# Performance work log

Hardware: AMD Instinct MI355X
Metric: run time of the kernel (lower is better)

Reference implementation:

```python
import jax, jax.numpy as jnp
import numpy as np

N_NODES = 100000
N_EDGES = 3200000
D = 128


def setup_inputs() -> dict:
    key = jax.random.key(0)
    ks = jax.random.split(key, 6)
    x = jax.random.normal(ks[0], (N_NODES, D), dtype=jnp.float32)
    w = jax.random.uniform(ks[1], (N_EDGES,), dtype=jnp.float32)
    W = jax.random.normal(ks[2], (D, D), dtype=jnp.float32) * (1.0 / np.sqrt(D))
    b = jax.random.normal(ks[3], (D,), dtype=jnp.float32) * 0.01
    src = jax.random.randint(ks[4], (N_EDGES,), 0, N_NODES, dtype=jnp.int64)
    dst = jax.random.randint(ks[5], (N_EDGES,), 0, N_NODES, dtype=jnp.int64)
    return {"x": x, "w": w, "W": W, "b": b, "src": src, "dst": dst}


def reference(x, w, W, b, src, dst):
    # h = linear(x)  -> [N, D]
    h = x @ W.T + b
    # u_mul_e: gather source features, scale by per-edge weight  -> [E, D]
    m = h[src] * w[:, None]
    # sum aggregation at destinations (SpMM scatter-add)  -> [N, D]
    out = jax.ops.segment_sum(m, dst, num_segments=N_NODES)
    return out
```

## Files before the change

kernel.cpp:

```cpp
#include <hip/hip_runtime.h>
#include <hip/hip_fp16.h>

constexpr int N_NODES = 100000;
constexpr int N_EDGES = 3200000;
constexpr int NB2 = (N_NODES + 63) >> 6;
constexpr int LCAP = 2432;
constexpr int TILE = 8192;
constexpr int NTILES = (N_EDGES + TILE - 1) / TILE;

__global__ __launch_bounds__(256) void cvt_kernel(const float* __restrict__ x,
                                                  __half* __restrict__ xh) {
  const int stride = gridDim.x * 256;
  const int total = N_NODES * 128 / 4;
  for (int i = blockIdx.x * 256 + threadIdx.x; i < total; i += stride) {
    float4 v = ((const float4*)x)[i];
    __half2 a = __floats2half2_rn(v.x, v.y);
    __half2 b = __floats2half2_rn(v.z, v.w);
    ((__half2*)xh)[2 * i] = a;
    ((__half2*)xh)[2 * i + 1] = b;
  }
}

__global__ __launch_bounds__(256) void bin3_kernel(
    const int* __restrict__ src, const int* __restrict__ dst,
    const float* __restrict__ w, int* __restrict__ gtail,
    int2* __restrict__ lists) {
  __shared__ int lcnt[NB2];
  __shared__ int lbase[NB2];
  const int t = threadIdx.x;
  const int e0 = blockIdx.x * TILE;
  const int n = min(TILE, N_EDGES - e0);

  for (int i = t; i < NB2; i += 256) lcnt[i] = 0;
  __syncthreads();

  for (int off = t; off < n; off += 256)
    atomicAdd(&lcnt[(dst[e0 + off] >> 6)], 1);
  __syncthreads();

  for (int i = t; i < NB2; i += 256) {
    int c = lcnt[i];
    lbase[i] = (c > 0) ? atomicAdd(&gtail[i], c) : 0;
    lcnt[i] = 0;
  }
  __syncthreads();

  for (int off = t; off < n; off += 256) {
    int e = e0 + off;
    int d = dst[e];
    int l = d >> 6;
    int p = lbase[l] + atomicAdd(&lcnt[l], 1);
    if ((unsigned)p < (unsigned)LCAP)
      lists[(size_t)l * LCAP + p] =
          make_int2(src[e] | ((d & 63) << 17), __float_as_int(w[e]));
  }
}

__global__ __launch_bounds__(256) void agg4_kernel(
    const __half* __restrict__ xh, const int2* __restrict__ lists,
    const int* __restrict__ gtail, float* __restrict__ agg_out,
    float* __restrict__ sw) {
  __shared__ int2 sorted[LCAP];
  __shared__ int rcnt[64], roff[65], rcur[64];
  const int b = blockIdx.x;
  const int t = threadIdx.x;
  const int c = min(gtail[b], LCAP);
  const int2* base = lists + (size_t)b * LCAP;

  if (t < 64) rcnt[t] = 0;
  __syncthreads();

  for (int j = t; j < c; j += 256)
    atomicAdd(&rcnt[(base[j].x >> 17) & 63], 1);
  __syncthreads();

  if (t < 64) {
    int v = rcnt[t];
    int inc = v;
    #pragma unroll
    for (int d = 1; d < 64; d <<= 1) {
      int u = __shfl_up(inc, d, 64);
      if (t >= d) inc += u;
    }
    roff[t] = inc - v;
    rcur[t] = inc - v;
    if (t == 63) roff[64] = inc;
  }
  __syncthreads();

  for (int j = t; j < c; j += 256) {
    int2 r = base[j];
    int p = atomicAdd(&rcur[(r.x >> 17) & 63], 1);
    if ((unsigned)p < (unsigned)LCAP) sorted[p] = r;
  }
  __syncthreads();

  const int wv = t >> 6, lane = t & 63;
  const int nd = min(64, N_NODES - b * 64);
  const __half2* xh2 = (const __half2*)xh;
  for (int ri = 0; ri < 16; ++ri) {
    int r = wv * 16 + ri;
    int j0 = min(roff[r], c), j1 = min(roff[r + 1], c);
    float2 acc = make_float2(0.f, 0.f);
    float sws = 0.f;
    int j = j0;
    for (; j + 8 <= j1; j += 8) {
      int2 e0 = sorted[j];
      int2 e1 = sorted[j + 1];
      int2 e2 = sorted[j + 2];
      int2 e3 = sorted[j + 3];
      int2 e4 = sorted[j + 4];
      int2 e5 = sorted[j + 5];
      int2 e6 = sorted[j + 6];
      int2 e7 = sorted[j + 7];
      __half2 h0 = xh2[(size_t)(e0.x & 0x1FFFF) * 64 + lane];
      __half2 h1 = xh2[(size_t)(e1.x & 0x1FFFF) * 64 + lane];
      __half2 h2 = xh2[(size_t)(e2.x & 0x1FFFF) * 64 + lane];
      __half2 h3 = xh2[(size_t)(e3.x & 0x1FFFF) * 64 + lane];
      __half2 h4 = xh2[(size_t)(e4.x & 0x1FFFF) * 64 + lane];
      __half2 h5 = xh2[(size_t)(e5.x & 0x1FFFF) * 64 + lane];
      __half2 h6 = xh2[(size_t)(e6.x & 0x1FFFF) * 64 + lane];
      __half2 h7 = xh2[(size_t)(e7.x & 0x1FFFF) * 64 + lane];
      float2 v0 = __half22float2(h0);
      float2 v1 = __half22float2(h1);
      float2 v2 = __half22float2(h2);
      float2 v3 = __half22float2(h3);
      float2 v4 = __half22float2(h4);
      float2 v5 = __half22float2(h5);
      float2 v6 = __half22float2(h6);
      float2 v7 = __half22float2(h7);
      float w0 = __int_as_float(e0.y), w1 = __int_as_float(e1.y);
      float w2 = __int_as_float(e2.y), w3 = __int_as_float(e3.y);
      float w4 = __int_as_float(e4.y), w5 = __int_as_float(e5.y);
      float w6 = __int_as_float(e6.y), w7 = __int_as_float(e7.y);
      acc.x = fmaf(w0, v0.x, acc.x); acc.y = fmaf(w0, v0.y, acc.y);
      acc.x = fmaf(w1, v1.x, acc.x); acc.y = fmaf(w1, v1.y, acc.y);
      acc.x = fmaf(w2, v2.x, acc.x); acc.y = fmaf(w2, v2.y, acc.y);
      acc.x = fmaf(w3, v3.x, acc.x); acc.y = fmaf(w3, v3.y, acc.y);
      acc.x = fmaf(w4, v4.x, acc.x); acc.y = fmaf(w4, v4.y, acc.y);
      acc.x = fmaf(w5, v5.x, acc.x); acc.y = fmaf(w5, v5.y, acc.y);
      acc.x = fmaf(w6, v6.x, acc.x); acc.y = fmaf(w6, v6.y, acc.y);
      acc.x = fmaf(w7, v7.x, acc.x); acc.y = fmaf(w7, v7.y, acc.y);
      sws += ((w0 + w1) + (w2 + w3)) + ((w4 + w5) + (w6 + w7));
    }
    for (; j < j1; ++j) {
      int2 e0 = sorted[j];
      float2 v0 = __half22float2(xh2[(size_t)(e0.x & 0x1FFFF) * 64 + lane]);
      float w0 = __int_as_float(e0.y);
      acc.x = fmaf(w0, v0.x, acc.x);
      acc.y = fmaf(w0, v0.y, acc.y);
      sws += w0;
    }
    if (r < nd) {
      ((float2*)agg_out)[(size_t)(b * 64 + r) * 64 + lane] = acc;
      if (lane == 0) sw[b * 64 + r] = sws;
    }
  }
}

__global__ __launch_bounds__(256, 2) void linear3_kernel(
    float* __restrict__ io, const float* __restrict__ W,
    const float* __restrict__ bias, const float* __restrict__ sw) {
  __shared__ float Wt[128][132];
  const int t = threadIdx.x;
  const int row0 = blockIdx.x * 64;

  #pragma unroll
  for (int i = 0; i < 16; ++i) {
    int f4 = t + 256 * i;
    int c = f4 >> 5;
    int k = (f4 & 31) * 4;
    float4 v = *(const float4*)(W + (size_t)c * 128 + k);
    Wt[k + 0][c] = v.x;
    Wt[k + 1][c] = v.y;
    Wt[k + 2][c] = v.z;
    Wt[k + 3][c] = v.w;
  }
  __syncthreads();

  const int tx = t & 15;
  const int ty = t >> 4;
  const float* xr[4];
  #pragma unroll
  for (int i = 0; i < 4; ++i) {
    int r = row0 + ty * 4 + i;
    xr[i] = (r < N_NODES) ? (io + (size_t)r * 128) : io;
  }

  float acc[4][8];
  #pragma unroll
  for (int i = 0; i < 4; ++i)
    #pragma unroll
    for (int j = 0; j < 8; ++j) acc[i][j] = 0.f;

  for (int k0 = 0; k0 < 128; k0 += 4) {
    float4 a[4];
    #pragma unroll
    for (int i = 0; i < 4; ++i) a[i] = *(const float4*)(xr[i] + k0);
    #pragma unroll
    for (int kk = 0; kk < 4; ++kk) {
      int k = k0 + kk;
      float4 b0 = *(const float4*)&Wt[k][tx * 8];
      float4 b1 = *(const float4*)&Wt[k][tx * 8 + 4];
      #pragma unroll
      for (int i = 0; i < 4; ++i) {
        float av = (kk == 0) ? a[i].x : (kk == 1) ? a[i].y
                  : (kk == 2) ? a[i].z : a[i].w;
        acc[i][0] = fmaf(av, b0.x, acc[i][0]);
        acc[i][1] = fmaf(av, b0.y, acc[i][1]);
        acc[i][2] = fmaf(av, b0.z, acc[i][2]);
        acc[i][3] = fmaf(av, b0.w, acc[i][3]);
        acc[i][4] = fmaf(av, b1.x, acc[i][4]);
        acc[i][5] = fmaf(av, b1.y, acc[i][5]);
        acc[i][6] = fmaf(av, b1.z, acc[i][6]);
        acc[i][7] = fmaf(av, b1.w, acc[i][7]);
      }
    }
  }

  float4 bb0 = *(const float4*)(bias + tx * 8);
  float4 bb1 = *(const float4*)(bias + tx * 8 + 4);
  #pragma unroll
  for (int i = 0; i < 4; ++i) {
    int r = row0 + ty * 4 + i;
    if (r < N_NODES) {
      float s = sw[r];
      float4 o0 = make_float4(acc[i][0] + s * bb0.x, acc[i][1] + s * bb0.y,
                              acc[i][2] + s * bb0.z, acc[i][3] + s * bb0.w);
      float4 o1 = make_float4(acc[i][4] + s * bb1.x, acc[i][5] + s * bb1.y,
                              acc[i][6] + s * bb1.z, acc[i][7] + s * bb1.w);
      float* orow = io + (size_t)r * 128 + tx * 8;
      *(float4*)orow = o0;
      *(float4*)(orow + 4) = o1;
    }
  }
}

extern "C" void kernel_launch(void* const* d_in, const int* in_sizes, int n_in,
                              void* d_out, int out_size, void* d_ws, size_t ws_size,
                              hipStream_t stream) {
  const float* x = (const float*)d_in[0];
  const float* w = (const float*)d_in[1];
  const float* W = (const float*)d_in[2];
  const float* bias = (const float*)d_in[3];
  const int* src = (const int*)d_in[4];
  const int* dst = (const int*)d_in[5];
  float* out = (float*)d_out;

  char* p = (char*)d_ws;
  __half* xh = (__half*)p;
  size_t o = (size_t)N_NODES * 128 * sizeof(__half);
  o = (o + 255) & ~(size_t)255;
  int2* lists = (int2*)(p + o);
  o += (size_t)NB2 * LCAP * sizeof(int2);
  int* gtail = (int*)(p + o);
  o += (size_t)NB2 * sizeof(int);
  o = (o + 255) & ~(size_t)255;
  float* sw = (float*)(p + o);

  hipMemsetAsync(gtail, 0, (size_t)NB2 * sizeof(int), stream);
  cvt_kernel<<<2048, 256, 0, stream>>>(x, xh);
  bin3_kernel<<<NTILES, 256, 0, stream>>>(src, dst, w, gtail, lists);
  agg4_kernel<<<NB2, 256, 0, stream>>>(xh, lists, gtail, out, sw);
  linear3_kernel<<<NB2, 256, 0, stream>>>(out, W, bias, sw);
}
```

Measured before the change: 414.6 us.

## Sort edges by source window and destination so concurrent blocks gather nearby rows

The aggregation kernel now bins each block's edges by a composite key of source-node window (src>>14) and destination row. It walks the windows in the outer loop, keeping all 16 per-row accumulators in registers. The aim is for concurrently running blocks to gather from the same source region at the same time, improving L2 locality of the half-precision feature gathers. The binning kernel also moves to 1024-thread blocks. The costs are more registers, a larger shared-memory histogram and scan, and a reduced inner unroll from 8 to 4.

```diff
diff --git a/kernel.cpp b/kernel.cpp
--- a/kernel.cpp
+++ b/kernel.cpp
@@ -7,6 +7,8 @@
 constexpr int LCAP = 2432;
 constexpr int TILE = 8192;
 constexpr int NTILES = (N_EDGES + TILE - 1) / TILE;
+constexpr int NWIN = 8;
+constexpr int NKEY = NWIN * 64;
 
 __global__ __launch_bounds__(256) void cvt_kernel(const float* __restrict__ x,
                                                   __half* __restrict__ xh) {
@@ -14,14 +16,12 @@
   const int total = N_NODES * 128 / 4;
   for (int i = blockIdx.x * 256 + threadIdx.x; i < total; i += stride) {
     float4 v = ((const float4*)x)[i];
-    __half2 a = __floats2half2_rn(v.x, v.y);
-    __half2 b = __floats2half2_rn(v.z, v.w);
-    ((__half2*)xh)[2 * i] = a;
-    ((__half2*)xh)[2 * i + 1] = b;
-  }
-}
-
-__global__ __launch_bounds__(256) void bin3_kernel(
+    ((__half2*)xh)[2 * i] = __floats2half2_rn(v.x, v.y);
+    ((__half2*)xh)[2 * i + 1] = __floats2half2_rn(v.z, v.w);
+  }
+}
+
+__global__ __launch_bounds__(1024) void bin4_kernel(
     const int* __restrict__ src, const int* __restrict__ dst,
     const float* __restrict__ w, int* __restrict__ gtail,
     int2* __restrict__ lists) {
@@ -31,21 +31,21 @@
   const int e0 = blockIdx.x * TILE;
   const int n = min(TILE, N_EDGES - e0);
 
-  for (int i = t; i < NB2; i += 256) lcnt[i] = 0;
-  __syncthreads();
-
-  for (int off = t; off < n; off += 256)
+  for (int i = t; i < NB2; i += 1024) lcnt[i] = 0;
+  __syncthreads();
+
+  for (int off = t; off < n; off += 1024)
     atomicAdd(&lcnt[(dst[e0 + off] >> 6)], 1);
   __syncthreads();
 
-  for (int i = t; i < NB2; i += 256) {
+  for (int i = t; i < NB2; i += 1024) {
     int c = lcnt[i];
     lbase[i] = (c > 0) ? atomicAdd(&gtail[i], c) : 0;
     lcnt[i] = 0;
   }
   __syncthreads();
 
-  for (int off = t; off < n; off += 256) {
+  for (int off = t; off < n; off += 1024) {
     int e = e0 + off;
     int d = dst[e];
     int l = d >> 6;
@@ -56,41 +56,54 @@
   }
 }
 
-__global__ __launch_bounds__(256) void agg4_kernel(
+__global__ __launch_bounds__(256) void agg5_kernel(
     const __half* __restrict__ xh, const int2* __restrict__ lists,
     const int* __restrict__ gtail, float* __restrict__ agg_out,
     float* __restrict__ sw) {
   __shared__ int2 sorted[LCAP];
-  __shared__ int rcnt[64], roff[65], rcur[64];
+  __shared__ int kcnt[NKEY];
+  __shared__ int koff[NKEY + 1];
+  __shared__ int kcur[NKEY];
   const int b = blockIdx.x;
   const int t = threadIdx.x;
   const int c = min(gtail[b], LCAP);
   const int2* base = lists + (size_t)b * LCAP;
 
-  if (t < 64) rcnt[t] = 0;
-  __syncthreads();
-
-  for (int j = t; j < c; j += 256)
-    atomicAdd(&rcnt[(base[j].x >> 17) & 63], 1);
+  for (int i = t; i < NKEY; i += 256) kcnt[i] = 0;
+  __syncthreads();
+
+  for (int j = t; j < c; j += 256) {
+    int rx = base[j].x;
+    int key = ((rx & 0x1FFFF) >> 14) * 64 + ((rx >> 17) & 63);
+    atomicAdd(&kcnt[key], 1);
+  }
   __syncthreads();
 
   if (t < 64) {
-    int v = rcnt[t];
-    int inc = v;
+    int base8 = t * 8;
+    int loc[8], run = 0;
+    #pragma unroll
+    for (int i = 0; i < 8; ++i) { loc[i] = run; run += kcnt[base8 + i]; }
+    int inc = run;
     #pragma unroll
     for (int d = 1; d < 64; d <<= 1) {
       int u = __shfl_up(inc, d, 64);
       if (t >= d) inc += u;
     }
-    roff[t] = inc - v;
-    rcur[t] = inc - v;
-    if (t == 63) roff[64] = inc;
+    int excl = inc - run;
+    #pragma unroll
+    for (int i = 0; i < 8; ++i) {
+      koff[base8 + i] = excl + loc[i];
+      kcur[base8 + i] = excl + loc[i];
+    }
+    if (t == 63) koff[NKEY] = inc;
   }
   __syncthreads();
 
   for (int j = t; j < c; j += 256) {
     int2 r = base[j];
-    int p = atomicAdd(&rcur[(r.x >> 17) & 63], 1);
+    int key = ((r.x & 0x1FFFF) >> 14) * 64 + ((r.x >> 17) & 63);
+    int p = atomicAdd(&kcur[key], 1);
     if ((unsigned)p < (unsigned)LCAP) sorted[p] = r;
   }
   __syncthreads();
@@ -98,62 +111,51 @@
   const int wv = t >> 6, lane = t & 63;
   const int nd = min(64, N_NODES - b * 64);
   const __half2* xh2 = (const __half2*)xh;
+  float2 acc[16];
+  float sws[16];
+  #pragma unroll
+  for (int i = 0; i < 16; ++i) { acc[i] = make_float2(0.f, 0.f); sws[i] = 0.f; }
+
+  for (int s = 0; s < NWIN; ++s) {
+    #pragma unroll
+    for (int ri = 0; ri < 16; ++ri) {
+      int key = s * 64 + wv * 16 + ri;
+      int j0 = min(koff[key], c), j1 = min(koff[key + 1], c);
+      int j = j0;
+      for (; j + 4 <= j1; j += 4) {
+        int2 e0 = sorted[j];
+        int2 e1 = sorted[j + 1];
+        int2 e2 = sorted[j + 2];
+        int2 e3 = sorted[j + 3];
+        float2 v0 = __half22float2(xh2[(size_t)(e0.x & 0x1FFFF) * 64 + lane]);
+        float2 v1 = __half22float2(xh2[(size_t)(e1.x & 0x1FFFF) * 64 + lane]);
+        float2 v2 = __half22float2(xh2[(size_t)(e2.x & 0x1FFFF) * 64 + lane]);
+        float2 v3 = __half22float2(xh2[(size_t)(e3.x & 0x1FFFF) * 64 + lane]);
+        float w0 = __int_as_float(e0.y), w1 = __int_as_float(e1.y);
+        float w2 = __int_as_float(e2.y), w3 = __int_as_float(e3.y);
+        acc[ri].x = fmaf(w0, v0.x, acc[ri].x); acc[ri].y = fmaf(w0, v0.y, acc[ri].y);
+        acc[ri].x = fmaf(w1, v1.x, acc[ri].x); acc[ri].y = fmaf(w1, v1.y, acc[ri].y);
+        acc[ri].x = fmaf(w2, v2.x, acc[ri].x); acc[ri].y = fmaf(w2, v2.y, acc[ri].y);
+        acc[ri].x = fmaf(w3, v3.x, acc[ri].x); acc[ri].y = fmaf(w3, v3.y, acc[ri].y);
+        sws[ri] += (w0 + w1) + (w2 + w3);
+      }
+      for (; j < j1; ++j) {
+        int2 e0 = sorted[j];
+        float2 v0 = __half22float2(xh2[(size_t)(e0.x & 0x1FFFF) * 64 + lane]);
+        float w0 = __int_as_float(e0.y);
+        acc[ri].x = fmaf(w0, v0.x, acc[ri].x);
+        acc[ri].y = fmaf(w0, v0.y, acc[ri].y);
+        sws[ri] += w0;
+      }
+    }
+  }
+
+  #pragma unroll
   for (int ri = 0; ri < 16; ++ri) {
     int r = wv * 16 + ri;
-    int j0 = min(roff[r], c), j1 = min(roff[r + 1], c);
-    float2 acc = make_float2(0.f, 0.f);
-    float sws = 0.f;
-    int j = j0;
-    for (; j + 8 <= j1; j += 8) {
-      int2 e0 = sorted[j];
-      int2 e1 = sorted[j + 1];
-      int2 e2 = sorted[j + 2];
-      int2 e3 = sorted[j + 3];
-      int2 e4 = sorted[j + 4];
-      int2 e5 = sorted[j + 5];
-      int2 e6 = sorted[j + 6];
-      int2 e7 = sorted[j + 7];
-      __half2 h0 = xh2[(size_t)(e0.x & 0x1FFFF) * 64 + lane];
-      __half2 h1 = xh2[(size_t)(e1.x & 0x1FFFF) * 64 + lane];
-      __half2 h2 = xh2[(size_t)(e2.x & 0x1FFFF) * 64 + lane];
-      __half2 h3 = xh2[(size_t)(e3.x & 0x1FFFF) * 64 + lane];
-      __half2 h4 = xh2[(size_t)(e4.x & 0x1FFFF) * 64 + lane];
-      __half2 h5 = xh2[(size_t)(e5.x & 0x1FFFF) * 64 + lane];
-      __half2 h6 = xh2[(size_t)(e6.x & 0x1FFFF) * 64 + lane];
-      __half2 h7 = xh2[(size_t)(e7.x & 0x1FFFF) * 64 + lane];
-      float2 v0 = __half22float2(h0);
-      float2 v1 = __half22float2(h1);
-      float2 v2 = __half22float2(h2);
-      float2 v3 = __half22float2(h3);
-      float2 v4 = __half22float2(h4);
-      float2 v5 = __half22float2(h5);
-      float2 v6 = __half22float2(h6);
-      float2 v7 = __half22float2(h7);
-      float w0 = __int_as_float(e0.y), w1 = __int_as_float(e1.y);
-      float w2 = __int_as_float(e2.y), w3 = __int_as_float(e3.y);
-      float w4 = __int_as_float(e4.y), w5 = __int_as_float(e5.y);
-      float w6 = __int_as_float(e6.y), w7 = __int_as_float(e7.y);
-      acc.x = fmaf(w0, v0.x, acc.x); acc.y = fmaf(w0, v0.y, acc.y);
-      acc.x = fmaf(w1, v1.x, acc.x); acc.y = fmaf(w1, v1.y, acc.y);
-      acc.x = fmaf(w2, v2.x, acc.x); acc.y = fmaf(w2, v2.y, acc.y);
-      acc.x = fmaf(w3, v3.x, acc.x); acc.y = fmaf(w3, v3.y, acc.y);
-      acc.x = fmaf(w4, v4.x, acc.x); acc.y = fmaf(w4, v4.y, acc.y);
-      acc.x = fmaf(w5, v5.x, acc.x); acc.y = fmaf(w5, v5.y, acc.y);
-      acc.x = fmaf(w6, v6.x, acc.x); acc.y = fmaf(w6, v6.y, acc.y);
-      acc.x = fmaf(w7, v7.x, acc.x); acc.y = fmaf(w7, v7.y, acc.y);
-      sws += ((w0 + w1) + (w2 + w3)) + ((w4 + w5) + (w6 + w7));
-    }
-    for (; j < j1; ++j) {
-      int2 e0 = sorted[j];
-      float2 v0 = __half22float2(xh2[(size_t)(e0.x & 0x1FFFF) * 64 + lane]);
-      float w0 = __int_as_float(e0.y);
-      acc.x = fmaf(w0, v0.x, acc.x);
-      acc.y = fmaf(w0, v0.y, acc.y);
-      sws += w0;
-    }
     if (r < nd) {
-      ((float2*)agg_out)[(size_t)(b * 64 + r) * 64 + lane] = acc;
-      if (lane == 0) sw[b * 64 + r] = sws;
+      ((float2*)agg_out)[(size_t)(b * 64 + r) * 64 + lane] = acc[ri];
+      if (lane == 0) sw[b * 64 + r] = sws[ri];
     }
   }
 }
@@ -260,7 +262,7 @@
 
   hipMemsetAsync(gtail, 0, (size_t)NB2 * sizeof(int), stream);
   cvt_kernel<<<2048, 256, 0, stream>>>(x, xh);
-  bin3_kernel<<<NTILES, 256, 0, stream>>>(src, dst, w, gtail, lists);
-  agg4_kernel<<<NB2, 256, 0, stream>>>(xh, lists, gtail, out, sw);
+  bin4_kernel<<<NTILES, 1024, 0, stream>>>(src, dst, w, gtail, lists);
+  agg5_kernel<<<NB2, 256, 0, stream>>>(xh, lists, gtail, out, sw);
   linear3_kernel<<<NB2, 256, 0, stream>>>(out, W, bias, sw);
 }
```

New measurement: 483.4 us. +16.6%, slower.

## Replace global-atomic bucket lists with per-tile local sort and offset matrix

Applied to the files above, without the earlier changes.

The binning kernel now counting-sorts each tile of 12500 edges by destination bucket entirely in shared memory, using 1024-thread blocks and a block-wide scan. It writes the records out contiguously plus a per-tile offset table. This removes the global tail atomics, the memset and the scattered writes into fixed-capacity lists. In the aggregation kernel, each of the 256 threads reads its own tile's small segment for the bucket, giving serial, poorly coalesced reads of about nine records per thread. The binning kernel uses roughly 112KB of shared memory per block, which limits occupancy.

```diff
diff --git a/kernel.cpp b/kernel.cpp
--- a/kernel.cpp
+++ b/kernel.cpp
@@ -5,8 +5,9 @@
 constexpr int N_EDGES = 3200000;
 constexpr int NB2 = (N_NODES + 63) >> 6;
 constexpr int LCAP = 2432;
-constexpr int TILE = 8192;
-constexpr int NTILES = (N_EDGES + TILE - 1) / TILE;
+constexpr int TILE2 = 12500;
+constexpr int NTILE2 = N_EDGES / TILE2;
+constexpr int LSTRIDE = NB2 + 1;
 
 __global__ __launch_bounds__(256) void cvt_kernel(const float* __restrict__ x,
                                                   __half* __restrict__ xh) {
@@ -14,64 +15,95 @@
   const int total = N_NODES * 128 / 4;
   for (int i = blockIdx.x * 256 + threadIdx.x; i < total; i += stride) {
     float4 v = ((const float4*)x)[i];
-    __half2 a = __floats2half2_rn(v.x, v.y);
-    __half2 b = __floats2half2_rn(v.z, v.w);
-    ((__half2*)xh)[2 * i] = a;
-    ((__half2*)xh)[2 * i + 1] = b;
-  }
-}
-
-__global__ __launch_bounds__(256) void bin3_kernel(
+    ((__half2*)xh)[2 * i] = __floats2half2_rn(v.x, v.y);
+    ((__half2*)xh)[2 * i + 1] = __floats2half2_rn(v.z, v.w);
+  }
+}
+
+__global__ __launch_bounds__(1024) void bint_kernel(
     const int* __restrict__ src, const int* __restrict__ dst,
-    const float* __restrict__ w, int* __restrict__ gtail,
-    int2* __restrict__ lists) {
+    const float* __restrict__ w, int2* __restrict__ recs,
+    int* __restrict__ loffm) {
+  __shared__ int2 rec[TILE2];
   __shared__ int lcnt[NB2];
-  __shared__ int lbase[NB2];
+  __shared__ int loff[NB2];
+  __shared__ int wsum[16];
   const int t = threadIdx.x;
-  const int e0 = blockIdx.x * TILE;
-  const int n = min(TILE, N_EDGES - e0);
-
-  for (int i = t; i < NB2; i += 256) lcnt[i] = 0;
-  __syncthreads();
-
-  for (int off = t; off < n; off += 256)
-    atomicAdd(&lcnt[(dst[e0 + off] >> 6)], 1);
-  __syncthreads();
-
-  for (int i = t; i < NB2; i += 256) {
-    int c = lcnt[i];
-    lbase[i] = (c > 0) ? atomicAdd(&gtail[i], c) : 0;
-    lcnt[i] = 0;
-  }
-  __syncthreads();
-
-  for (int off = t; off < n; off += 256) {
-    int e = e0 + off;
+  const int e0 = blockIdx.x * TILE2;
+
+  for (int i = t; i < NB2; i += 1024) lcnt[i] = 0;
+  __syncthreads();
+
+  for (int i = t; i < TILE2; i += 1024)
+    atomicAdd(&lcnt[dst[e0 + i] >> 6], 1);
+  __syncthreads();
+
+  {
+    int i0 = 2 * t, i1 = 2 * t + 1;
+    int c0 = (i0 < NB2) ? lcnt[i0] : 0;
+    int c1 = (i1 < NB2) ? lcnt[i1] : 0;
+    int v = c0 + c1;
+    int inc = v;
+    #pragma unroll
+    for (int d = 1; d < 64; d <<= 1) {
+      int u = __shfl_up(inc, d, 64);
+      if ((t & 63) >= d) inc += u;
+    }
+    if ((t & 63) == 63) wsum[t >> 6] = inc;
+    __syncthreads();
+    if (t < 16) {
+      int s = wsum[t];
+      int inc2 = s;
+      #pragma unroll
+      for (int d = 1; d < 16; d <<= 1) {
+        int u = __shfl_up(inc2, d, 64);
+        if (t >= d) inc2 += u;
+      }
+      wsum[t] = inc2 - s;
+    }
+    __syncthreads();
+    int excl = (inc - v) + wsum[t >> 6];
+    if (i0 < NB2) loff[i0] = excl;
+    if (i1 < NB2) loff[i1] = excl + c0;
+  }
+  __syncthreads();
+
+  for (int i = t; i < NB2; i += 1024) lcnt[i] = loff[i];
+  __syncthreads();
+
+  for (int i = t; i < TILE2; i += 1024) {
+    int e = e0 + i;
     int d = dst[e];
     int l = d >> 6;
-    int p = lbase[l] + atomicAdd(&lcnt[l], 1);
-    if ((unsigned)p < (unsigned)LCAP)
-      lists[(size_t)l * LCAP + p] =
-          make_int2(src[e] | ((d & 63) << 17), __float_as_int(w[e]));
-  }
-}
-
-__global__ __launch_bounds__(256) void agg4_kernel(
-    const __half* __restrict__ xh, const int2* __restrict__ lists,
-    const int* __restrict__ gtail, float* __restrict__ agg_out,
+    int p = atomicAdd(&lcnt[l], 1);
+    rec[p] = make_int2(src[e] | ((d & 63) << 17), __float_as_int(w[e]));
+  }
+  __syncthreads();
+
+  for (int q = t; q < TILE2; q += 1024) recs[(size_t)e0 + q] = rec[q];
+  for (int i = t; i < NB2; i += 1024)
+    loffm[(size_t)blockIdx.x * LSTRIDE + i] = loff[i];
+  if (t == 0) loffm[(size_t)blockIdx.x * LSTRIDE + NB2] = TILE2;
+}
+
+__global__ __launch_bounds__(256) void agg8_kernel(
+    const __half* __restrict__ xh, const int2* __restrict__ recs,
+    const int* __restrict__ loffm, float* __restrict__ agg_out,
     float* __restrict__ sw) {
   __shared__ int2 sorted[LCAP];
   __shared__ int rcnt[64], roff[65], rcur[64];
   const int b = blockIdx.x;
   const int t = threadIdx.x;
-  const int c = min(gtail[b], LCAP);
-  const int2* base = lists + (size_t)b * LCAP;
+
+  const int j0 = loffm[(size_t)t * LSTRIDE + b];
+  const int j1 = loffm[(size_t)t * LSTRIDE + b + 1];
+  const int2* seg = recs + (size_t)t * TILE2;
 
   if (t < 64) rcnt[t] = 0;
   __syncthreads();
 
-  for (int j = t; j < c; j += 256)
-    atomicAdd(&rcnt[(base[j].x >> 17) & 63], 1);
+  for (int j = j0; j < j1; ++j)
+    atomicAdd(&rcnt[(seg[j].x >> 17) & 63], 1);
   __syncthreads();
 
   if (t < 64) {
@@ -88,8 +120,8 @@
   }
   __syncthreads();
 
-  for (int j = t; j < c; j += 256) {
-    int2 r = base[j];
+  for (int j = j0; j < j1; ++j) {
+    int2 r = seg[j];
     int p = atomicAdd(&rcur[(r.x >> 17) & 63], 1);
     if ((unsigned)p < (unsigned)LCAP) sorted[p] = r;
   }
@@ -100,11 +132,11 @@
   const __half2* xh2 = (const __half2*)xh;
   for (int ri = 0; ri < 16; ++ri) {
     int r = wv * 16 + ri;
-    int j0 = min(roff[r], c), j1 = min(roff[r + 1], c);
+    int s0 = min(roff[r], LCAP), s1 = min(roff[r + 1], LCAP);
     float2 acc = make_float2(0.f, 0.f);
     float sws = 0.f;
-    int j = j0;
-    for (; j + 8 <= j1; j += 8) {
+    int j = s0;
+    for (; j + 8 <= s1; j += 8) {
       int2 e0 = sorted[j];
       int2 e1 = sorted[j + 1];
       int2 e2 = sorted[j + 2];
@@ -143,7 +175,7 @@
       acc.x = fmaf(w7, v7.x, acc.x); acc.y = fmaf(w7, v7.y, acc.y);
       sws += ((w0 + w1) + (w2 + w3)) + ((w4 + w5) + (w6 + w7));
     }
-    for (; j < j1; ++j) {
+    for (; j < s1; ++j) {
       int2 e0 = sorted[j];
       float2 v0 = __half22float2(xh2[(size_t)(e0.x & 0x1FFFF) * 64 + lane]);
       float w0 = __int_as_float(e0.y);
@@ -251,16 +283,16 @@
   __half* xh = (__half*)p;
   size_t o = (size_t)N_NODES * 128 * sizeof(__half);
   o = (o + 255) & ~(size_t)255;
-  int2* lists = (int2*)(p + o);
-  o += (size_t)NB2 * LCAP * sizeof(int2);
-  int* gtail = (int*)(p + o);
-  o += (size_t)NB2 * sizeof(int);
+  int2* recs = (int2*)(p + o);
+  o += (size_t)N_EDGES * sizeof(int2);
+  o = (o + 255) & ~(size_t)255;
+  int* loffm = (int*)(p + o);
+  o += (size_t)NTILE2 * LSTRIDE * sizeof(int);
   o = (o + 255) & ~(size_t)255;
   float* sw = (float*)(p + o);
 
-  hipMemsetAsync(gtail, 0, (size_t)NB2 * sizeof(int), stream);
   cvt_kernel<<<2048, 256, 0, stream>>>(x, xh);
-  bin3_kernel<<<NTILES, 256, 0, stream>>>(src, dst, w, gtail, lists);
-  agg4_kernel<<<NB2, 256, 0, stream>>>(xh, lists, gtail, out, sw);
+  bint_kernel<<<NTILE2, 1024, 0, stream>>>(src, dst, w, recs, loffm);
+  agg8_kernel<<<NB2, 256, 0, stream>>>(xh, recs, loffm, out, sw);
   linear3_kernel<<<NB2, 256, 0, stream>>>(out, W, bias, sw);
 }
```

Result: slower. 427.3 us (+3.1%).
